# Optimization experiments

Hardware: AMD Instinct MI355X
Metric: run time of the kernel (lower is better)

## Reference

```python
import jax, jax.numpy as jnp
import numpy as np
import math

B, S, D, H, L, K = 4, 2048, 256, 8, 2, 3  # batch, seq, dim, heads, MTA layers, conv kernel
HS = D // H
EPS = 1e-6


def layer_norm(x, g, b):
    m = jnp.mean(x, axis=-1, keepdims=True)
    v = jnp.mean((x - m) ** 2, axis=-1, keepdims=True)
    return (x - m) * jax.lax.rsqrt(v + EPS) * g + b


def temporal_encoder(x, W, b):
    # x: [B,S,D]; W: [L,K,D,D] (WIO), b: [L,D]. Stack of kernel-3 'SAME' Conv1d, GELU between.
    for i in range(L):
        x = jax.lax.conv_general_dilated(
            x, W[i], window_strides=(1,), padding=[(1, 1)],
            dimension_numbers=("NWC", "WIO", "NWC")) + b[i]
        if i < L - 1:
            x = jax.nn.gelu(x)
    return x


def setup_inputs() -> dict:
    key = jax.random.key(0)
    ks = jax.random.split(key, 10)
    w = lambda k, shape: jax.random.normal(k, shape, jnp.float32) * 0.02
    return {
        "x": jax.random.normal(ks[0], (B, S, D), jnp.float32),
        "ln1_g": jnp.ones((D,), jnp.float32), "ln1_b": jnp.zeros((D,), jnp.float32),
        "Wq": w(ks[1], (L, K, D, D)), "bq": jnp.zeros((L, D), jnp.float32),
        "Wk": w(ks[2], (L, K, D, D)), "bk": jnp.zeros((L, D), jnp.float32),
        "Wv": w(ks[3], (L, K, D, D)), "bv": jnp.zeros((L, D), jnp.float32),
        "ln2_g": jnp.ones((D,), jnp.float32), "ln2_b": jnp.zeros((D,), jnp.float32),
        "Wo1": w(ks[4], (D, D)), "bo1": jnp.zeros((D,), jnp.float32),
        "Wo2": w(ks[5], (D, D)), "bo2": jnp.zeros((D,), jnp.float32),
        "mask": jax.random.randint(ks[6], (B, S), 0, 2).astype(jnp.int32),
    }


def reference(x, ln1_g, ln1_b, Wq, bq, Wk, bk, Wv, bv, ln2_g, ln2_b, Wo1, bo1, Wo2, bo2, mask):
    b_, s_ = x.shape[0], x.shape[1]
    h = layer_norm(x, ln1_g, ln1_b)
    q = temporal_encoder(h, Wq, bq).reshape(b_, s_, H, HS)
    k = temporal_encoder(h, Wk, bk).reshape(b_, s_, H, HS)
    v = temporal_encoder(h, Wv, bv).reshape(b_, s_, H, HS)
    # attention scores [B,H,S,S]
    scores = jnp.einsum("bqhd,bkhd->bhqk", q, k) / math.sqrt(HS)
    m = mask[:, None, None, :].astype(scores.dtype)  # [B,1,1,S]
    scores = scores + (1.0 - m) * (-1e30)
    probs = jax.nn.softmax(scores, axis=-1)
    attn = jnp.einsum("bhqk,bkhd->bqhd", probs, v).reshape(b_, s_, D)
    residual = x + attn  # dropout p=0
    o = layer_norm(residual, ln2_g, ln2_b)
    o = jax.nn.gelu(o @ Wo1 + bo1)  # 1x1 Conv1D == per-token linear
    o = o @ Wo2 + bo2 + residual
    return o
```

## Files before the change

kernel.cpp:

```cpp
#include <hip/hip_runtime.h>
#include <hip/hip_bf16.h>
#include <math.h>

#define BB 4
#define SS 2048
#define DD 256
#define HH 8
#define HSZ 32

typedef __attribute__((ext_vector_type(8))) short short8;
typedef __attribute__((ext_vector_type(4))) float f32x4;

__device__ __forceinline__ void gload_lds16(const void* g, void* l) {
    __builtin_amdgcn_global_load_lds((const unsigned int*)g, (unsigned int*)l,
                                     16, 0, 0);
}

__device__ __forceinline__ float exp2_hw(float x) {
    float r;
    asm("v_exp_f32 %0, %1" : "=v"(r) : "v"(x));
    return r;
}

__device__ __forceinline__ unsigned int perm_pack(float a, float b, unsigned int sel) {
    unsigned int r;
    asm("v_perm_b32 %0, %1, %2, %3"
        : "=v"(r)
        : "v"(__float_as_uint(b)), "v"(__float_as_uint(a)), "s"(sel));
    return r;
}

__device__ __forceinline__ float gelu_f(float x) {
    float x3 = x * x * x;
    float z = 0.7978845608028654f * fmaf(0.044715f, x3, x);
    float e = __expf(2.0f * z);
    float t = 1.0f - 2.0f / (e + 1.0f);
    return 0.5f * x * (1.0f + t);
}

__device__ __forceinline__ unsigned short f2bf(float f) {
    unsigned int u = __float_as_uint(f);
    u = (u + 0x7fffu + ((u >> 16) & 1u)) >> 16;
    return (unsigned short)u;
}

template<bool HASRES>
__device__ __forceinline__ void ln_wave_body(
    int t, int lane,
    const float* __restrict__ x, const float* __restrict__ addin,
    const float* __restrict__ g, const float* __restrict__ bvec,
    float* __restrict__ resid_out, unsigned short* __restrict__ oln_bf)
{
    const int base = t * DD + lane * 4;
    float4 v4 = *(const float4*)&x[base];
    if (HASRES) {
        float4 a4 = *(const float4*)&addin[base];
        v4.x += a4.x; v4.y += a4.y; v4.z += a4.z; v4.w += a4.w;
        *(float4*)&resid_out[base] = v4;
    }
    float s = (v4.x + v4.y) + (v4.z + v4.w);
    #pragma unroll
    for (int o = 1; o < 64; o <<= 1) s += __shfl_xor(s, o);
    float mean = s * (1.0f / 256.0f);
    float dx = v4.x - mean, dy = v4.y - mean, dz = v4.z - mean, dw = v4.w - mean;
    float q = (dx * dx + dy * dy) + (dz * dz + dw * dw);
    #pragma unroll
    for (int o = 1; o < 64; o <<= 1) q += __shfl_xor(q, o);
    float r = rsqrtf(q * (1.0f / 256.0f) + 1e-6f);
    const float4 g4 = *(const float4*)&g[lane * 4];
    const float4 b4 = *(const float4*)&bvec[lane * 4];
    ushort4 o4;
    o4.x = f2bf(dx * r * g4.x + b4.x);
    o4.y = f2bf(dy * r * g4.y + b4.y);
    o4.z = f2bf(dz * r * g4.z + b4.z);
    o4.w = f2bf(dw * r * g4.w + b4.w);
    *(ushort4*)&oln_bf[base] = o4;
}

__global__ __launch_bounds__(256) void prep_kernel(
    const float* __restrict__ Wq, const float* __restrict__ Wk,
    const float* __restrict__ Wv, const float* __restrict__ Wo1,
    const float* __restrict__ Wo2, unsigned short* __restrict__ wt,
    const float* __restrict__ x, const float* __restrict__ ln1g,
    const float* __restrict__ ln1b, unsigned short* __restrict__ h_bf,
    const int* __restrict__ mask, float* __restrict__ maskf)
{
    if (blockIdx.x < 1280) {
        const int WCp = 3 * DD * DD;
        const int WMp = DD * DD;
        const float* src; unsigned short* dst; int rel;
        int i = blockIdx.x;
        if (i < 1152) {
            int seg = i / 192; rel = i % 192;
            src = seg == 0 ? Wq : seg == 1 ? Wq + WCp : seg == 2 ? Wk :
                  seg == 3 ? Wk + WCp : seg == 4 ? Wv : Wv + WCp;
            dst = wt + (size_t)seg * WCp;
        } else {
            int j = i - 1152; int seg = j / 64; rel = j % 64;
            src = seg == 0 ? Wo1 : Wo2;
            dst = wt + (size_t)6 * WCp + (size_t)seg * WMp;
        }
        __shared__ unsigned short t[32][33];
        const int tx = threadIdx.x & 31, ty = threadIdx.x >> 5;
        const int r0 = (rel / 8) * 32, c0 = (rel % 8) * 32;
        #pragma unroll
        for (int j = 0; j < 32; j += 8)
            t[ty + j][tx] = f2bf(src[(r0 + ty + j) * 256 + c0 + tx]);
        __syncthreads();
        #pragma unroll
        for (int j = 0; j < 32; j += 8) {
            unsigned int och = (unsigned int)(c0 + ty + j);
            unsigned int k   = (unsigned int)(r0 + tx);
            unsigned int u   = och * 32u + (k & 31u);
            u ^= ((u >> 6) & 7u) << 3;
            dst[(size_t)(k >> 5) * 8192 + u] = t[tx][ty + j];
        }
    } else if (blockIdx.x < 3328) {
        const int wv = threadIdx.x >> 6, lane = threadIdx.x & 63;
        ln_wave_body<false>((blockIdx.x - 1280) * 4 + wv, lane,
                            x, nullptr, ln1g, ln1b, nullptr, h_bf);
    } else {
        const float M_ON  = -8.0f * 1.4426950408889634f;
        const float M_OFF = -1.442695e30f;
        int i = (blockIdx.x - 3328) * 1024 + threadIdx.x * 4;
        int4 m4 = *(const int4*)&mask[i];
        float4 f4;
        f4.x = m4.x ? M_ON : M_OFF;
        f4.y = m4.y ? M_ON : M_OFF;
        f4.z = m4.z ? M_ON : M_OFF;
        f4.w = m4.w ? M_ON : M_OFF;
        *(float4*)&maskf[i] = f4;
    }
}

__global__ __launch_bounds__(256, 3) void convdual_kernel(
    const unsigned short* __restrict__ in,
    const unsigned short* __restrict__ W0a, const unsigned short* __restrict__ W0b,
    const unsigned short* __restrict__ W0c,
    const unsigned short* __restrict__ W1a, const unsigned short* __restrict__ W1b,
    const unsigned short* __restrict__ W1c,
    const float* __restrict__ ba, const float* __restrict__ bb,
    const float* __restrict__ bc,
    unsigned short* __restrict__ oQ, unsigned short* __restrict__ oK,
    unsigned short* __restrict__ oV, int S)
{
    constexpr int LDW = 264;
    __shared__ __align__(16) unsigned short stage[36 * LDW];
    __shared__ __align__(16) unsigned short wbuf[2][8192];

    unsigned short* const inter = stage;

    const int set = blockIdx.x % 3;
    const int tile = blockIdx.x / 3;
    const unsigned short* W0 = set == 0 ? W0a : (set == 1 ? W0b : W0c);
    const unsigned short* W1 = set == 0 ? W1a : (set == 1 ? W1b : W1c);
    const float* bias         = set == 0 ? ba  : (set == 1 ? bb  : bc);
    unsigned short* outp      = set == 0 ? oQ  : (set == 1 ? oK  : oV);

    const int tid = threadIdx.x;
    const int lane = tid & 63, wv = tid >> 6;
    const int lm = lane & 15, lq = lane >> 4;
    const int tpb = S / 32;
    const int b = tile / tpb;
    const int s0 = (tile % tpb) * 32;
    const int NC = S / 32;
    const int c = s0 >> 5;

    for (int i = tid; i < 36 * 32; i += 256) {
        int r = i >> 5, c8 = (i & 31) << 3;
        int s = s0 + r - 2;
        int4 val = make_int4(0, 0, 0, 0);
        if (s >= 0 && s < S)
            val = *(const int4*)&in[(size_t)(b * S + s) * 256 + c8];
        *(int4*)&stage[r * LDW + c8] = val;
    }

    const int n0 = wv * 64;

    const int wq = wv * 4096;
    const char* w0p = (const char*)W0 + wq + lane * 16;
    const char* w1p = (const char*)W1 + wq + lane * 16;
    char* const wb0 = (char*)wbuf;

    unsigned int boff[4];
    #pragma unroll
    for (int nt = 0; nt < 4; ++nt) {
        unsigned int och = (unsigned int)(n0 + nt * 16 + lm);
        unsigned int R = och * 64u + (unsigned int)lq * 16u;
        boff[nt] = R ^ (((R >> 7) & 7u) << 4);
    }

    __syncthreads();

    {
        f32x4 acc[3][4];
        #pragma unroll
        for (int mt = 0; mt < 3; ++mt)
            #pragma unroll
            for (int nt = 0; nt < 4; ++nt) acc[mt][nt] = (f32x4){0.f, 0.f, 0.f, 0.f};

        #pragma unroll
        for (int j = 0; j < 4; ++j) gload_lds16(w0p + j * 1024,         wb0 + wq + j * 1024);
        #pragma unroll
        for (int j = 0; j < 4; ++j) gload_lds16(w0p + 16384 + j * 1024, wb0 + 16384 + wq + j * 1024);

        short8 a0c, a1c, a2c;
        {
            const int icc0 = lq * 8;
            int r20 = 32 + lm; r20 = r20 > 35 ? 35 : r20;
            a0c = *(const short8*)&stage[lm * LDW + icc0];
            a1c = *(const short8*)&stage[(16 + lm) * LDW + icc0];
            a2c = *(const short8*)&stage[r20 * LDW + icc0];
        }

        asm volatile("s_waitcnt vmcnt(4)" ::: "memory");
        __builtin_amdgcn_sched_barrier(0);
        short8 bfc[4];
        #pragma unroll
        for (int nt = 0; nt < 4; ++nt)
            bfc[nt] = *(const short8*)(wb0 + boff[nt]);

        #pragma unroll
        for (int it = 0; it < 24; ++it) {
            asm volatile("s_waitcnt lgkmcnt(0)" ::: "memory");
            __builtin_amdgcn_sched_barrier(0);
            if (it + 2 < 24) {
                char* ld = wb0 + ((it & 1) << 14) + wq;
                const int soff = (it + 2) * 16384;
                #pragma unroll
                for (int j = 0; j < 4; ++j)
                    gload_lds16(w0p + soff + j * 1024, ld + j * 1024);
            }
            __builtin_amdgcn_sched_barrier(0);

            __builtin_amdgcn_s_setprio(1);
            #pragma unroll
            for (int nt = 0; nt < 4; ++nt) {
                acc[0][nt] = __builtin_amdgcn_mfma_f32_16x16x32_bf16(a0c, bfc[nt], acc[0][nt], 0, 0, 0);
                acc[1][nt] = __builtin_amdgcn_mfma_f32_16x16x32_bf16(a1c, bfc[nt], acc[1][nt], 0, 0, 0);
                acc[2][nt] = __builtin_amdgcn_mfma_f32_16x16x32_bf16(a2c, bfc[nt], acc[2][nt], 0, 0, 0);
            }
            __builtin_amdgcn_s_setprio(0);
            __builtin_amdgcn_sched_barrier(0);

            if (it + 1 < 24) {
                if (it + 2 < 24) { asm volatile("s_waitcnt vmcnt(4)" ::: "memory"); }
                else             { asm volatile("s_waitcnt vmcnt(0)" ::: "memory"); }
                __builtin_amdgcn_sched_barrier(0);
                const char* wb = wb0 + (((it + 1) & 1) << 14);
                #pragma unroll
                for (int nt = 0; nt < 4; ++nt)
                    bfc[nt] = *(const short8*)(wb + boff[nt]);
                const int kk = (it + 1) >> 3;
                const int icc = ((it + 1) & 7) * 32 + lq * 8;
                int r2 = kk + 32 + lm; r2 = r2 > 35 ? 35 : r2;
                a0c = *(const short8*)&stage[(kk + lm) * LDW + icc];
                a1c = *(const short8*)&stage[(kk + 16 + lm) * LDW + icc];
                a2c = *(const short8*)&stage[r2 * LDW + icc];
            }
        }

        __syncthreads();

        #pragma unroll
        for (int j = 0; j < 4; ++j) gload_lds16(w1p + j * 1024,         wb0 + wq + j * 1024);
        #pragma unroll
        for (int j = 0; j < 4; ++j) gload_lds16(w1p + 16384 + j * 1024, wb0 + 16384 + wq + j * 1024);

        #pragma unroll
        for (int mt = 0; mt < 3; ++mt)
            #pragma unroll
            for (int nt = 0; nt < 4; ++nt) {
                int ch = n0 + nt * 16 + lm;
                float bv = bias[ch];
                #pragma unroll
                for (int r = 0; r < 4; ++r) {
                    int j = mt * 16 + lq * 4 + r;
                    if (j < 34) {
                        int token = s0 - 1 + j;
                        unsigned short v = (token >= 0 && token < S)
                            ? f2bf(gelu_f(acc[mt][nt][r] + bv)) : (unsigned short)0;
                        inter[j * LDW + ch] = v;
                    }
                }
            }
    }
    __syncthreads();

    f32x4 acc2[2][4];
    #pragma unroll
    for (int mt = 0; mt < 2; ++mt)
        #pragma unroll
        for (int nt = 0; nt < 4; ++nt) acc2[mt][nt] = (f32x4){0.f, 0.f, 0.f, 0.f};
    {
        char* const wb0 = (char*)wbuf;
        short8 a0c, a1c;
        {
            const int icc0 = lq * 8;
            a0c = *(const short8*)&inter[lm * LDW + icc0];
            a1c = *(const short8*)&inter[(16 + lm) * LDW + icc0];
        }

        asm volatile("s_waitcnt vmcnt(4)" ::: "memory");
        __builtin_amdgcn_sched_barrier(0);
        short8 bfc[4];
        #pragma unroll
        for (int nt = 0; nt < 4; ++nt)
            bfc[nt] = *(const short8*)(wb0 + boff[nt]);

        #pragma unroll
        for (int it = 0; it < 24; ++it) {
            asm volatile("s_waitcnt lgkmcnt(0)" ::: "memory");
            __builtin_amdgcn_sched_barrier(0);
            if (it + 2 < 24) {
                char* ld = wb0 + ((it & 1) << 14) + wq;
                const int soff = (it + 2) * 16384;
                #pragma unroll
                for (int j = 0; j < 4; ++j)
                    gload_lds16(w1p + soff + j * 1024, ld + j * 1024);
            }
            __builtin_amdgcn_sched_barrier(0);

            __builtin_amdgcn_s_setprio(1);
            #pragma unroll
            for (int nt = 0; nt < 4; ++nt) {
                acc2[0][nt] = __builtin_amdgcn_mfma_f32_16x16x32_bf16(a0c, bfc[nt], acc2[0][nt], 0, 0, 0);
                acc2[1][nt] = __builtin_amdgcn_mfma_f32_16x16x32_bf16(a1c, bfc[nt], acc2[1][nt], 0, 0, 0);
            }
            __builtin_amdgcn_s_setprio(0);
            __builtin_amdgcn_sched_barrier(0);

            if (it + 1 < 24) {
                if (it + 2 < 24) { asm volatile("s_waitcnt vmcnt(4)" ::: "memory"); }
                else             { asm volatile("s_waitcnt vmcnt(0)" ::: "memory"); }
                __builtin_amdgcn_sched_barrier(0);
                const char* wb = wb0 + (((it + 1) & 1) << 14);
                #pragma unroll
                for (int nt = 0; nt < 4; ++nt)
                    bfc[nt] = *(const short8*)(wb + boff[nt]);
                const int kk = (it + 1) >> 3;
                const int icc = ((it + 1) & 7) * 32 + lq * 8;
                a0c = *(const short8*)&inter[(kk + lm) * LDW + icc];
                a1c = *(const short8*)&inter[(kk + 16 + lm) * LDW + icc];
            }
        }
    }

    __syncthreads();
    if (set < 2) {
        #pragma unroll
        for (int mt = 0; mt < 2; ++mt)
            #pragma unroll
            for (int nt = 0; nt < 4; ++nt) {
                int o = n0 + nt * 16 + lm;
                int d = o & 31, h = o >> 5;
                float bv = bias[256 + o];
                #pragma unroll
                for (int r = 0; r < 4; ++r) {
                    int t = lq * 4 + r;
                    stage[mt * 4096 + (h * 64 + (d >> 3) * 16 + t) * 8 + (d & 7)] =
                        f2bf(acc2[mt][nt][r] + bv);
                }
            }
        __syncthreads();
        int h = tid >> 5;
        size_t base = ((size_t)(b * 8 + h) * NC + c) * 1024;
        #pragma unroll
        for (int half = 0; half < 2; ++half) {
            int4 v0 = *(const int4*)&stage[half * 4096 + tid * 16];
            int4 v1 = *(const int4*)&stage[half * 4096 + tid * 16 + 8];
            size_t dst = base + half * 512 + (tid & 31) * 16;
            *(int4*)&outp[dst] = v0;
            *(int4*)&outp[dst + 8] = v1;
        }
    } else {
        #pragma unroll
        for (int mt = 0; mt < 2; ++mt)
            #pragma unroll
            for (int nt = 0; nt < 4; ++nt) {
                int o = n0 + nt * 16 + lm;
                int d = o & 31, h = o >> 5;
                float bv = bias[256 + o];
                #pragma unroll
                for (int r = 0; r < 4; ++r) {
                    int t = lq * 4 + r;
                    stage[mt * 4096 +
                          ((h * 2 + (d >> 4)) * 32 + (t >> 3) * 16 + (d & 15)) * 8 + (t & 7)] =
                        f2bf(acc2[mt][nt][r] + bv);
                }
            }
        __syncthreads();
        int h = tid >> 5, dh = (tid >> 4) & 1;
        size_t base = ((size_t)(b * 8 + h) * NC + c) * 1024;
        #pragma unroll
        for (int half = 0; half < 2; ++half) {
            int4 v0 = *(const int4*)&stage[half * 4096 + tid * 16];
            int4 v1 = *(const int4*)&stage[half * 4096 + tid * 16 + 8];
            size_t dst = base + dh * 512 + half * 256 + (tid & 15) * 16;
            *(int4*)&outp[dst] = v0;
            *(int4*)&outp[dst + 8] = v1;
        }
    }
}

__global__ __launch_bounds__(256, 2) void tail_kernel(
    const float* __restrict__ x, const float* __restrict__ attn,
    const float* __restrict__ g2, const float* __restrict__ b2,
    const unsigned short* __restrict__ W1, const float* __restrict__ bo1,
    const unsigned short* __restrict__ W2, const float* __restrict__ bo2,
    float* __restrict__ out, int S)
{
    constexpr int LDW = 264;
    __shared__ __align__(16) unsigned short h_lds[16 * LDW];
    __shared__ __align__(16) unsigned short h2_lds[16 * LDW];
    __shared__ __align__(16) float resid_lds[16][DD];
    __shared__ __align__(16) unsigned short wbuf[2][8192];

    const int tid = threadIdx.x;
    const int lane = tid & 63, wv = tid >> 6;
    const int lm = lane & 15, lq = lane >> 4;
    const int t0 = blockIdx.x * 16;
    const int n0 = wv * 64;

    const int wq = wv * 4096;
    const char* w1p = (const char*)W1 + wq + lane * 16;
    const char* w2p = (const char*)W2 + wq + lane * 16;
    char* const wb0 = (char*)wbuf;

    unsigned int boff[4];
    #pragma unroll
    for (int nt = 0; nt < 4; ++nt) {
        unsigned int och = (unsigned int)(n0 + nt * 16 + lm);
        unsigned int R = och * 64u + (unsigned int)lq * 16u;
        boff[nt] = R ^ (((R >> 7) & 7u) << 4);
    }

    #pragma unroll
    for (int j = 0; j < 4; ++j) gload_lds16(w1p + j * 1024,         wb0 + wq + j * 1024);
    #pragma unroll
    for (int j = 0; j < 4; ++j) gload_lds16(w1p + 16384 + j * 1024, wb0 + 16384 + wq + j * 1024);

    #pragma unroll
    for (int j = 0; j < 4; ++j) {
        int t = wv * 4 + j;
        int base = (t0 + t) * DD + lane * 4;
        float4 v4 = *(const float4*)&x[base];
        float4 a4 = *(const float4*)&attn[base];
        v4.x += a4.x; v4.y += a4.y; v4.z += a4.z; v4.w += a4.w;
        *(float4*)&resid_lds[t][lane * 4] = v4;
        float s = (v4.x + v4.y) + (v4.z + v4.w);
        #pragma unroll
        for (int o = 1; o < 64; o <<= 1) s += __shfl_xor(s, o);
        float mean = s * (1.0f / 256.0f);
        float dx = v4.x - mean, dy = v4.y - mean, dz = v4.z - mean, dw = v4.w - mean;
        float q = (dx * dx + dy * dy) + (dz * dz + dw * dw);
        #pragma unroll
        for (int o = 1; o < 64; o <<= 1) q += __shfl_xor(q, o);
        float r = rsqrtf(q * (1.0f / 256.0f) + 1e-6f);
        const float4 g4 = *(const float4*)&g2[lane * 4];
        const float4 b4 = *(const float4*)&b2[lane * 4];
        ushort4 o4;
        o4.x = f2bf(dx * r * g4.x + b4.x);
        o4.y = f2bf(dy * r * g4.y + b4.y);
        o4.z = f2bf(dz * r * g4.z + b4.z);
        o4.w = f2bf(dw * r * g4.w + b4.w);
        *(ushort4*)&h_lds[t * LDW + lane * 4] = o4;
    }
    __syncthreads();

    {
        f32x4 acc[4];
        #pragma unroll
        for (int nt = 0; nt < 4; ++nt) acc[nt] = (f32x4){0.f, 0.f, 0.f, 0.f};

        short8 a0c = *(const short8*)&h_lds[lm * LDW + lq * 8];
        asm volatile("s_waitcnt vmcnt(4)" ::: "memory");
        __builtin_amdgcn_sched_barrier(0);
        short8 bfc[4];
        #pragma unroll
        for (int nt = 0; nt < 4; ++nt)
            bfc[nt] = *(const short8*)(wb0 + boff[nt]);

        #pragma unroll
        for (int it = 0; it < 8; ++it) {
            asm volatile("s_waitcnt lgkmcnt(0)" ::: "memory");
            __builtin_amdgcn_sched_barrier(0);
            if (it + 2 < 8) {
                char* ld = wb0 + ((it & 1) << 14) + wq;
                const int soff = (it + 2) * 16384;
                #pragma unroll
                for (int j = 0; j < 4; ++j)
                    gload_lds16(w1p + soff + j * 1024, ld + j * 1024);
            }
            __builtin_amdgcn_sched_barrier(0);

            __builtin_amdgcn_s_setprio(1);
            #pragma unroll
            for (int nt = 0; nt < 4; ++nt)
                acc[nt] = __builtin_amdgcn_mfma_f32_16x16x32_bf16(a0c, bfc[nt], acc[nt], 0, 0, 0);
            __builtin_amdgcn_s_setprio(0);
            __builtin_amdgcn_sched_barrier(0);

            if (it + 1 < 8) {
                if (it + 2 < 8) { asm volatile("s_waitcnt vmcnt(4)" ::: "memory"); }
                else            { asm volatile("s_waitcnt vmcnt(0)" ::: "memory"); }
                __builtin_amdgcn_sched_barrier(0);
                const char* wb = wb0 + (((it + 1) & 1) << 14);
                #pragma unroll
                for (int nt = 0; nt < 4; ++nt)
                    bfc[nt] = *(const short8*)(wb + boff[nt]);
                a0c = *(const short8*)&h_lds[lm * LDW + (it + 1) * 32 + lq * 8];
            }
        }

        asm volatile("s_waitcnt lgkmcnt(0)" ::: "memory");
        __builtin_amdgcn_sched_barrier(0);
        #pragma unroll
        for (int j = 0; j < 4; ++j) gload_lds16(w2p + j * 1024,         wb0 + wq + j * 1024);
        #pragma unroll
        for (int j = 0; j < 4; ++j) gload_lds16(w2p + 16384 + j * 1024, wb0 + 16384 + wq + j * 1024);

        #pragma unroll
        for (int nt = 0; nt < 4; ++nt) {
            int ch = n0 + nt * 16 + lm;
            float bv = bo1[ch];
            #pragma unroll
            for (int r = 0; r < 4; ++r) {
                int tok = lq * 4 + r;
                h2_lds[tok * LDW + ch] = f2bf(gelu_f(acc[nt][r] + bv));
            }
        }
    }
    __syncthreads();

    {
        f32x4 acc[4];
        #pragma unroll
        for (int nt = 0; nt < 4; ++nt) acc[nt] = (f32x4){0.f, 0.f, 0.f, 0.f};

        short8 a0c = *(const short8*)&h2_lds[lm * LDW + lq * 8];
        asm volatile("s_waitcnt vmcnt(4)" ::: "memory");
        __builtin_amdgcn_sched_barrier(0);
        short8 bfc[4];
        #pragma unroll
        for (int nt = 0; nt < 4; ++nt)
            bfc[nt] = *(const short8*)(wb0 + boff[nt]);

        #pragma unroll
        for (int it = 0; it < 8; ++it) {
            asm volatile("s_waitcnt lgkmcnt(0)" ::: "memory");
            __builtin_amdgcn_sched_barrier(0);
            if (it + 2 < 8) {
                char* ld = wb0 + ((it & 1) << 14) + wq;
                const int soff = (it + 2) * 16384;
                #pragma unroll
                for (int j = 0; j < 4; ++j)
                    gload_lds16(w2p + soff + j * 1024, ld + j * 1024);
            }
            __builtin_amdgcn_sched_barrier(0);

            __builtin_amdgcn_s_setprio(1);
            #pragma unroll
            for (int nt = 0; nt < 4; ++nt)
                acc[nt] = __builtin_amdgcn_mfma_f32_16x16x32_bf16(a0c, bfc[nt], acc[nt], 0, 0, 0);
            __builtin_amdgcn_s_setprio(0);
            __builtin_amdgcn_sched_barrier(0);

            if (it + 1 < 8) {
                if (it + 2 < 8) { asm volatile("s_waitcnt vmcnt(4)" ::: "memory"); }
                else            { asm volatile("s_waitcnt vmcnt(0)" ::: "memory"); }
                __builtin_amdgcn_sched_barrier(0);
                const char* wb = wb0 + (((it + 1) & 1) << 14);
                #pragma unroll
                for (int nt = 0; nt < 4; ++nt)
                    bfc[nt] = *(const short8*)(wb + boff[nt]);
                a0c = *(const short8*)&h2_lds[lm * LDW + (it + 1) * 32 + lq * 8];
            }
        }
        #pragma unroll
        for (int nt = 0; nt < 4; ++nt) {
            int ch = n0 + nt * 16 + lm;
            float bv = bo2[ch];
            #pragma unroll
            for (int r = 0; r < 4; ++r) {
                int tok = lq * 4 + r;
                out[(size_t)(t0 + tok) * DD + ch] = acc[nt][r] + bv + resid_lds[tok][ch];
            }
        }
    }
}

__global__ __launch_bounds__(256) void attn_mfma_kernel(
    const unsigned short* __restrict__ Qf, const unsigned short* __restrict__ Kf,
    const unsigned short* __restrict__ Vf, const float* __restrict__ maskf,
    float* __restrict__ Out, int S, int H)
{
    constexpr int LDP = 40;
    __shared__ __align__(16) unsigned short p_lds[4][16 * LDP];

    const int bh = ((blockIdx.x & 7) << 2) | ((blockIdx.x >> 3) & 3);
    const int qt = (blockIdx.x >> 5) * 64;
    const int b = bh / H;
    const int tid = threadIdx.x;
    const int lane = tid & 63, wv = tid >> 6;
    const int lm = lane & 15, lq = lane >> 4;
    const int q0 = qt + wv * 16;
    const int NC = S / 32;

    const size_t base = (size_t)bh * NC * 1024;
    short8 qfrag = *(const short8*)&Qf[base + (size_t)(q0 >> 5) * 1024
                                      + ((q0 >> 4) & 1) * 512 + lane * 8];
    const unsigned short* kp = Kf + base + lane * 8;
    const unsigned short* vp = Vf + base + lane * 8;

    short8 ones;
    #pragma unroll
    for (int j = 0; j < 8; ++j) ones[j] = (short)0x3F80;

    f32x4 o0 = {0.f, 0.f, 0.f, 0.f}, o1 = {0.f, 0.f, 0.f, 0.f};
    f32x4 lacc = {0.f, 0.f, 0.f, 0.f};
    const f32x4 zf = {0.f, 0.f, 0.f, 0.f};

    const float scale2 = 0.17677669529663687f * 1.4426950408889634f;
    const unsigned int psel = 0x07060302u;
    const float* mp0 = maskf + b * S + lq * 4;
    const float* mp1 = mp0 + 16;

    unsigned short* pw = p_lds[wv];
    const int pst = lm * LDP + lq * 4;
    const int prd = lm * LDP + lq * 8;

    short8 kA0 = *(const short8*)(kp);
    short8 kA1 = *(const short8*)(kp + 512);
    short8 vA0 = *(const short8*)(vp);
    short8 vA1 = *(const short8*)(vp + 512);
    short8 kB0, kB1, vB0, vB1;

    for (int c = 0; c < NC; c += 2) {
        {
            const unsigned short* kq = kp + (size_t)(c + 1) * 1024;
            const unsigned short* vq = vp + (size_t)(c + 1) * 1024;
            kB0 = *(const short8*)(kq);
            kB1 = *(const short8*)(kq + 512);
            vB0 = *(const short8*)(vq);
            vB1 = *(const short8*)(vq + 512);
        }

        {
            f32x4 s0 = __builtin_amdgcn_mfma_f32_16x16x32_bf16(kA0, qfrag, zf, 0, 0, 0);
            f32x4 s1 = __builtin_amdgcn_mfma_f32_16x16x32_bf16(kA1, qfrag, zf, 0, 0, 0);

            float4 mf0 = *(const float4*)(mp0 + c * 32);
            float4 mf1 = *(const float4*)(mp1 + c * 32);

            float p[8];
            p[0] = exp2_hw(fmaf(s0[0], scale2, mf0.x));
            p[1] = exp2_hw(fmaf(s0[1], scale2, mf0.y));
            p[2] = exp2_hw(fmaf(s0[2], scale2, mf0.z));
            p[3] = exp2_hw(fmaf(s0[3], scale2, mf0.w));
            p[4] = exp2_hw(fmaf(s1[0], scale2, mf1.x));
            p[5] = exp2_hw(fmaf(s1[1], scale2, mf1.y));
            p[6] = exp2_hw(fmaf(s1[2], scale2, mf1.z));
            p[7] = exp2_hw(fmaf(s1[3], scale2, mf1.w));

            uint2 w0, w1;
            w0.x = perm_pack(p[0], p[1], psel); w0.y = perm_pack(p[2], p[3], psel);
            w1.x = perm_pack(p[4], p[5], psel); w1.y = perm_pack(p[6], p[7], psel);
            *(uint2*)&pw[pst] = w0;
            *(uint2*)&pw[pst + 16] = w1;

            short8 pA = *(const short8*)&pw[prd];

            lacc = __builtin_amdgcn_mfma_f32_16x16x32_bf16(pA, ones, lacc, 0, 0, 0);
            o0   = __builtin_amdgcn_mfma_f32_16x16x32_bf16(pA, vA0, o0, 0, 0, 0);
            o1   = __builtin_amdgcn_mfma_f32_16x16x32_bf16(pA, vA1, o1, 0, 0, 0);
        }

        if (c + 2 < NC) {
            const unsigned short* kq = kp + (size_t)(c + 2) * 1024;
            const unsigned short* vq = vp + (size_t)(c + 2) * 1024;
            kA0 = *(const short8*)(kq);
            kA1 = *(const short8*)(kq + 512);
            vA0 = *(const short8*)(vq);
            vA1 = *(const short8*)(vq + 512);
        }

        {
            f32x4 s0 = __builtin_amdgcn_mfma_f32_16x16x32_bf16(kB0, qfrag, zf, 0, 0, 0);
            f32x4 s1 = __builtin_amdgcn_mfma_f32_16x16x32_bf16(kB1, qfrag, zf, 0, 0, 0);

            float4 mf0 = *(const float4*)(mp0 + (c + 1) * 32);
            float4 mf1 = *(const float4*)(mp1 + (c + 1) * 32);

            float p[8];
            p[0] = exp2_hw(fmaf(s0[0], scale2, mf0.x));
            p[1] = exp2_hw(fmaf(s0[1], scale2, mf0.y));
            p[2] = exp2_hw(fmaf(s0[2], scale2, mf0.z));
            p[3] = exp2_hw(fmaf(s0[3], scale2, mf0.w));
            p[4] = exp2_hw(fmaf(s1[0], scale2, mf1.x));
            p[5] = exp2_hw(fmaf(s1[1], scale2, mf1.y));
            p[6] = exp2_hw(fmaf(s1[2], scale2, mf1.z));
            p[7] = exp2_hw(fmaf(s1[3], scale2, mf1.w));

            uint2 w0, w1;
            w0.x = perm_pack(p[0], p[1], psel); w0.y = perm_pack(p[2], p[3], psel);
            w1.x = perm_pack(p[4], p[5], psel); w1.y = perm_pack(p[6], p[7], psel);
            *(uint2*)&pw[pst] = w0;
            *(uint2*)&pw[pst + 16] = w1;

            short8 pA = *(const short8*)&pw[prd];

            lacc = __builtin_amdgcn_mfma_f32_16x16x32_bf16(pA, ones, lacc, 0, 0, 0);
            o0   = __builtin_amdgcn_mfma_f32_16x16x32_bf16(pA, vB0, o0, 0, 0, 0);
            o1   = __builtin_amdgcn_mfma_f32_16x16x32_bf16(pA, vB1, o1, 0, 0, 0);
        }
    }

    #pragma unroll
    for (int r = 0; r < 4; ++r) {
        float inv = 1.0f / lacc[r];
        size_t ob = (size_t)(b * S + q0 + lq * 4 + r) * 256 + (bh % H) * 32;
        Out[ob + lm] = o0[r] * inv;
        Out[ob + 16 + lm] = o1[r] * inv;
    }
}

extern "C" void kernel_launch(void* const* d_in, const int* in_sizes, int n_in,
                              void* d_out, int out_size, void* d_ws, size_t ws_size,
                              hipStream_t stream) {
    (void)in_sizes; (void)n_in; (void)out_size; (void)ws_size;
    const float* x    = (const float*)d_in[0];
    const float* ln1g = (const float*)d_in[1];
    const float* ln1b = (const float*)d_in[2];
    const float* Wq   = (const float*)d_in[3];
    const float* bq   = (const float*)d_in[4];
    const float* Wk   = (const float*)d_in[5];
    const float* bk   = (const float*)d_in[6];
    const float* Wv   = (const float*)d_in[7];
    const float* bv   = (const float*)d_in[8];
    const float* ln2g = (const float*)d_in[9];
    const float* ln2b = (const float*)d_in[10];
    const float* Wo1  = (const float*)d_in[11];
    const float* bo1  = (const float*)d_in[12];
    const float* Wo2  = (const float*)d_in[13];
    const float* bo2  = (const float*)d_in[14];
    const int*   mask = (const int*)d_in[15];
    float* out = (float*)d_out;

    const int S = SS, H = HH;
    const int T = BB * SS;
    const size_t NE = (size_t)T * DD;
    float* ws    = (float*)d_ws;
    float* attn  = ws + 0 * NE;
    float* maskf = ws + 1 * NE;
    unsigned short* qf_g  = (unsigned short*)(ws + 2 * NE);
    unsigned short* kf_g  = qf_g + NE;
    unsigned short* h_bf  = kf_g + NE;
    unsigned short* wt    = h_bf + NE;
    const int WC = 3 * DD * DD;
    const int WM = DD * DD;
    unsigned short* wtq0 = wt;
    unsigned short* wtq1 = wt + WC;
    unsigned short* wtk0 = wt + 2 * WC;
    unsigned short* wtk1 = wt + 3 * WC;
    unsigned short* wtv0 = wt + 4 * WC;
    unsigned short* wtv1 = wt + 5 * WC;
    unsigned short* wto1 = wt + 6 * WC;
    unsigned short* wto2 = wt + 6 * WC + WM;
    unsigned short* vf_g = wt + 6 * WC + 2 * WM;

    prep_kernel<<<1280 + T / 4 + 8, 256, 0, stream>>>(
        Wq, Wk, Wv, Wo1, Wo2, wt, x, ln1g, ln1b, h_bf, mask, maskf);

    convdual_kernel<<<(T / 32) * 3, 256, 0, stream>>>(
        h_bf, wtq0, wtk0, wtv0, wtq1, wtk1, wtv1, bq, bk, bv,
        qf_g, kf_g, vf_g, S);

    attn_mfma_kernel<<<BB * H * (S / 64), 256, 0, stream>>>(qf_g, kf_g, vf_g, maskf, attn, S, H);

    tail_kernel<<<T / 16, 256, 0, stream>>>(
        x, attn, ln2g, ln2b, wto1, bo1, wto2, bo2, out, S);
}
```

Measured before the change: 192.8 us.

## Process four query tiles per wave to reuse K/V fragments in attention

Each wave in the attention kernel now handles 64 queries (four 16-row tiles) instead of 16, so every loaded K/V fragment and mask value is reused across four score/PV MFMA groups. The grid shrinks fourfold, to 256 blocks, and launch bounds now request one block per SIMD. This cuts global K/V load traffic per unit of work and gives more independent MFMAs to interleave. In exchange it uses more registers and LDS, and the smaller grid may underfill the GPU's compute units.

```diff
diff --git a/kernel.cpp b/kernel.cpp
--- a/kernel.cpp
+++ b/kernel.cpp
@@ -590,26 +590,30 @@
     }
 }
 
-__global__ __launch_bounds__(256) void attn_mfma_kernel(
+__global__ __launch_bounds__(256, 1) void attn_mfma_kernel(
     const unsigned short* __restrict__ Qf, const unsigned short* __restrict__ Kf,
     const unsigned short* __restrict__ Vf, const float* __restrict__ maskf,
     float* __restrict__ Out, int S, int H)
 {
     constexpr int LDP = 40;
-    __shared__ __align__(16) unsigned short p_lds[4][16 * LDP];
+    __shared__ __align__(16) unsigned short p_lds[4][4][16 * LDP];
 
     const int bh = ((blockIdx.x & 7) << 2) | ((blockIdx.x >> 3) & 3);
-    const int qt = (blockIdx.x >> 5) * 64;
+    const int qt = (blockIdx.x >> 5) * 256;
     const int b = bh / H;
     const int tid = threadIdx.x;
     const int lane = tid & 63, wv = tid >> 6;
     const int lm = lane & 15, lq = lane >> 4;
-    const int q0 = qt + wv * 16;
+    const int q0 = qt + wv * 64;
     const int NC = S / 32;
 
     const size_t base = (size_t)bh * NC * 1024;
-    short8 qfrag = *(const short8*)&Qf[base + (size_t)(q0 >> 5) * 1024
-                                      + ((q0 >> 4) & 1) * 512 + lane * 8];
+    const unsigned short* qp = &Qf[base + (size_t)(q0 >> 5) * 1024 + lane * 8];
+    short8 qf[4];
+    qf[0] = *(const short8*)(qp);
+    qf[1] = *(const short8*)(qp + 512);
+    qf[2] = *(const short8*)(qp + 1024);
+    qf[3] = *(const short8*)(qp + 1536);
     const unsigned short* kp = Kf + base + lane * 8;
     const unsigned short* vp = Vf + base + lane * 8;
 
@@ -617,8 +621,13 @@
     #pragma unroll
     for (int j = 0; j < 8; ++j) ones[j] = (short)0x3F80;
 
-    f32x4 o0 = {0.f, 0.f, 0.f, 0.f}, o1 = {0.f, 0.f, 0.f, 0.f};
-    f32x4 lacc = {0.f, 0.f, 0.f, 0.f};
+    f32x4 o0[4], o1[4], lacc[4];
+    #pragma unroll
+    for (int qn = 0; qn < 4; ++qn) {
+        o0[qn] = (f32x4){0.f, 0.f, 0.f, 0.f};
+        o1[qn] = (f32x4){0.f, 0.f, 0.f, 0.f};
+        lacc[qn] = (f32x4){0.f, 0.f, 0.f, 0.f};
+    }
     const f32x4 zf = {0.f, 0.f, 0.f, 0.f};
 
     const float scale2 = 0.17677669529663687f * 1.4426950408889634f;
@@ -626,9 +635,43 @@
     const float* mp0 = maskf + b * S + lq * 4;
     const float* mp1 = mp0 + 16;
 
-    unsigned short* pw = p_lds[wv];
     const int pst = lm * LDP + lq * 4;
     const int prd = lm * LDP + lq * 8;
+
+    auto chunk_body = [&](short8 k0, short8 k1, short8 v0, short8 v1, int c) {
+        f32x4 s0[4], s1[4];
+        #pragma unroll
+        for (int qn = 0; qn < 4; ++qn) {
+            s0[qn] = __builtin_amdgcn_mfma_f32_16x16x32_bf16(k0, qf[qn], zf, 0, 0, 0);
+            s1[qn] = __builtin_amdgcn_mfma_f32_16x16x32_bf16(k1, qf[qn], zf, 0, 0, 0);
+        }
+        float4 mf0 = *(const float4*)(mp0 + c * 32);
+        float4 mf1 = *(const float4*)(mp1 + c * 32);
+        #pragma unroll
+        for (int qn = 0; qn < 4; ++qn) {
+            float p[8];
+            p[0] = exp2_hw(fmaf(s0[qn][0], scale2, mf0.x));
+            p[1] = exp2_hw(fmaf(s0[qn][1], scale2, mf0.y));
+            p[2] = exp2_hw(fmaf(s0[qn][2], scale2, mf0.z));
+            p[3] = exp2_hw(fmaf(s0[qn][3], scale2, mf0.w));
+            p[4] = exp2_hw(fmaf(s1[qn][0], scale2, mf1.x));
+            p[5] = exp2_hw(fmaf(s1[qn][1], scale2, mf1.y));
+            p[6] = exp2_hw(fmaf(s1[qn][2], scale2, mf1.z));
+            p[7] = exp2_hw(fmaf(s1[qn][3], scale2, mf1.w));
+            uint2 w0, w1;
+            w0.x = perm_pack(p[0], p[1], psel); w0.y = perm_pack(p[2], p[3], psel);
+            w1.x = perm_pack(p[4], p[5], psel); w1.y = perm_pack(p[6], p[7], psel);
+            *(uint2*)&p_lds[wv][qn][pst] = w0;
+            *(uint2*)&p_lds[wv][qn][pst + 16] = w1;
+        }
+        #pragma unroll
+        for (int qn = 0; qn < 4; ++qn) {
+            short8 pA = *(const short8*)&p_lds[wv][qn][prd];
+            lacc[qn] = __builtin_amdgcn_mfma_f32_16x16x32_bf16(pA, ones, lacc[qn], 0, 0, 0);
+            o0[qn]   = __builtin_amdgcn_mfma_f32_16x16x32_bf16(pA, v0, o0[qn], 0, 0, 0);
+            o1[qn]   = __builtin_amdgcn_mfma_f32_16x16x32_bf16(pA, v1, o1[qn], 0, 0, 0);
+        }
+    };
 
     short8 kA0 = *(const short8*)(kp);
     short8 kA1 = *(const short8*)(kp + 512);
@@ -646,35 +689,7 @@
             vB1 = *(const short8*)(vq + 512);
         }
 
-        {
-            f32x4 s0 = __builtin_amdgcn_mfma_f32_16x16x32_bf16(kA0, qfrag, zf, 0, 0, 0);
-            f32x4 s1 = __builtin_amdgcn_mfma_f32_16x16x32_bf16(kA1, qfrag, zf, 0, 0, 0);
-
-            float4 mf0 = *(const float4*)(mp0 + c * 32);
-            float4 mf1 = *(const float4*)(mp1 + c * 32);
-
-            float p[8];
-            p[0] = exp2_hw(fmaf(s0[0], scale2, mf0.x));
-            p[1] = exp2_hw(fmaf(s0[1], scale2, mf0.y));
-            p[2] = exp2_hw(fmaf(s0[2], scale2, mf0.z));
-            p[3] = exp2_hw(fmaf(s0[3], scale2, mf0.w));
-            p[4] = exp2_hw(fmaf(s1[0], scale2, mf1.x));
-            p[5] = exp2_hw(fmaf(s1[1], scale2, mf1.y));
-            p[6] = exp2_hw(fmaf(s1[2], scale2, mf1.z));
-            p[7] = exp2_hw(fmaf(s1[3], scale2, mf1.w));
-
-            uint2 w0, w1;
-            w0.x = perm_pack(p[0], p[1], psel); w0.y = perm_pack(p[2], p[3], psel);
-            w1.x = perm_pack(p[4], p[5], psel); w1.y = perm_pack(p[6], p[7], psel);
-            *(uint2*)&pw[pst] = w0;
-            *(uint2*)&pw[pst + 16] = w1;
-
-            short8 pA = *(const short8*)&pw[prd];
-
-            lacc = __builtin_amdgcn_mfma_f32_16x16x32_bf16(pA, ones, lacc, 0, 0, 0);
-            o0   = __builtin_amdgcn_mfma_f32_16x16x32_bf16(pA, vA0, o0, 0, 0, 0);
-            o1   = __builtin_amdgcn_mfma_f32_16x16x32_bf16(pA, vA1, o1, 0, 0, 0);
-        }
+        chunk_body(kA0, kA1, vA0, vA1, c);
 
         if (c + 2 < NC) {
             const unsigned short* kq = kp + (size_t)(c + 2) * 1024;
@@ -685,44 +700,18 @@
             vA1 = *(const short8*)(vq + 512);
         }
 
-        {
-            f32x4 s0 = __builtin_amdgcn_mfma_f32_16x16x32_bf16(kB0, qfrag, zf, 0, 0, 0);
-            f32x4 s1 = __builtin_amdgcn_mfma_f32_16x16x32_bf16(kB1, qfrag, zf, 0, 0, 0);
-
-            float4 mf0 = *(const float4*)(mp0 + (c + 1) * 32);
-            float4 mf1 = *(const float4*)(mp1 + (c + 1) * 32);
-
-            float p[8];
-            p[0] = exp2_hw(fmaf(s0[0], scale2, mf0.x));
-            p[1] = exp2_hw(fmaf(s0[1], scale2, mf0.y));
-            p[2] = exp2_hw(fmaf(s0[2], scale2, mf0.z));
-            p[3] = exp2_hw(fmaf(s0[3], scale2, mf0.w));
-            p[4] = exp2_hw(fmaf(s1[0], scale2, mf1.x));
-            p[5] = exp2_hw(fmaf(s1[1], scale2, mf1.y));
-            p[6] = exp2_hw(fmaf(s1[2], scale2, mf1.z));
-            p[7] = exp2_hw(fmaf(s1[3], scale2, mf1.w));
-
-            uint2 w0, w1;
-            w0.x = perm_pack(p[0], p[1], psel); w0.y = perm_pack(p[2], p[3], psel);
-            w1.x = perm_pack(p[4], p[5], psel); w1.y = perm_pack(p[6], p[7], psel);
-            *(uint2*)&pw[pst] = w0;
-            *(uint2*)&pw[pst + 16] = w1;
-
-            short8 pA = *(const short8*)&pw[prd];
-
-            lacc = __builtin_amdgcn_mfma_f32_16x16x32_bf16(pA, ones, lacc, 0, 0, 0);
-            o0   = __builtin_amdgcn_mfma_f32_16x16x32_bf16(pA, vB0, o0, 0, 0, 0);
-            o1   = __builtin_amdgcn_mfma_f32_16x16x32_bf16(pA, vB1, o1, 0, 0, 0);
-        }
-    }
-
-    #pragma unroll
-    for (int r = 0; r < 4; ++r) {
-        float inv = 1.0f / lacc[r];
-        size_t ob = (size_t)(b * S + q0 + lq * 4 + r) * 256 + (bh % H) * 32;
-        Out[ob + lm] = o0[r] * inv;
-        Out[ob + 16 + lm] = o1[r] * inv;
-    }
+        chunk_body(kB0, kB1, vB0, vB1, c + 1);
+    }
+
+    #pragma unroll
+    for (int qn = 0; qn < 4; ++qn)
+        #pragma unroll
+        for (int r = 0; r < 4; ++r) {
+            float inv = 1.0f / lacc[qn][r];
+            size_t ob = (size_t)(b * S + q0 + qn * 16 + lq * 4 + r) * 256 + (bh % H) * 32;
+            Out[ob + lm] = o0[qn][r] * inv;
+            Out[ob + 16 + lm] = o1[qn][r] * inv;
+        }
 }
 
 extern "C" void kernel_launch(void* const* d_in, const int* in_sizes, int n_in,
@@ -776,7 +765,7 @@
         h_bf, wtq0, wtk0, wtv0, wtq1, wtk1, wtv1, bq, bk, bv,
         qf_g, kf_g, vf_g, S);
 
-    attn_mfma_kernel<<<BB * H * (S / 64), 256, 0, stream>>>(qf_g, kf_g, vf_g, maskf, attn, S, H);
+    attn_mfma_kernel<<<BB * H * (S / 256), 256, 0, stream>>>(qf_g, kf_g, vf_g, maskf, attn, S, H);
 
     tail_kernel<<<T / 16, 256, 0, stream>>>(
         x, attn, ln2g, ln2b, wto1, bo1, wto2, bo2, out, S);
```

Measured after the change: 191.5 us. No clear change (-0.7%).
